# Kernel optimization log

Hardware: AMD Instinct MI355X
Metric: run time of the kernel (lower is better)

The kernel has to match this reference:

```python
import jax, jax.numpy as jnp
import numpy as np

D_MODEL = 1024
N_HEADS = 16
D_K = D_MODEL // N_HEADS
THETA = 10000.0
BATCH, SEQ = 4, 2048


def apply_rope(x, pos, theta=THETA):
    # x: [B, H, S, d_k]; pos: [S] int. Rotate interleaved pairs (x_{2i}, x_{2i+1}).
    half = x.shape[-1] // 2
    inv_freq = theta ** (-jnp.arange(half, dtype=x.dtype) * 2.0 / x.shape[-1])  # [half]
    ang = pos.astype(x.dtype)[:, None] * inv_freq[None, :]                      # [S, half]
    cos, sin = jnp.cos(ang), jnp.sin(ang)
    x1, x2 = x[..., 0::2], x[..., 1::2]
    r1 = x1 * cos - x2 * sin
    r2 = x1 * sin + x2 * cos
    return jnp.stack([r1, r2], axis=-1).reshape(x.shape)


def setup_inputs() -> dict:
    key = jax.random.key(0)
    k1, k2, k3 = jax.random.split(key, 3)
    x = jax.random.normal(k1, (BATCH, SEQ, D_MODEL), dtype=jnp.float32)
    W_qkv = jax.random.normal(k2, (3 * D_MODEL, D_MODEL), dtype=jnp.float32) * (D_MODEL ** -0.5)
    b_qkv = jnp.zeros((3 * D_MODEL,), dtype=jnp.float32)
    W_o = jax.random.normal(k3, (D_MODEL, D_MODEL), dtype=jnp.float32) * (D_MODEL ** -0.5)
    b_o = jnp.zeros((D_MODEL,), dtype=jnp.float32)
    token_positions = jnp.arange(SEQ, dtype=jnp.int64 if jax.config.jax_enable_x64 else jnp.int32)
    return {"x": x, "token_positions": token_positions, "W_qkv": W_qkv,
            "b_qkv": b_qkv, "W_o": W_o, "b_o": b_o}


def reference(x, token_positions, W_qkv, b_qkv, W_o, b_o):
    B, S, _ = x.shape
    qkv = x @ W_qkv.T + b_qkv                                   # [B, S, 3*d_model]
    qkv = qkv.reshape(B, S, 3, N_HEADS, D_K)
    qkv = jnp.transpose(qkv, (2, 0, 3, 1, 4))                   # [3, B, H, S, d_k]
    q, k, v = qkv[0], qkv[1], qkv[2]
    q = apply_rope(q, token_positions)
    k = apply_rope(k, token_positions)
    scores = jnp.einsum('bhqd,bhkd->bhqk', q / jnp.sqrt(jnp.asarray(D_K, x.dtype)), k)
    causal = jnp.tril(jnp.ones((S, S), dtype=bool))             # True where attended
    scores = jnp.where(causal, scores, jnp.asarray(-jnp.inf, scores.dtype))
    attn = jax.nn.softmax(scores, axis=-1)
    out = jnp.einsum('bhqk,bhkd->bhqd', attn, v)                # [B, H, S, d_k]
    out = jnp.transpose(out, (0, 2, 1, 3)).reshape(B, S, D_MODEL)
    return out @ W_o.T + b_o
```

## Files before the change

kernel.cpp:

```cpp
#include <hip/hip_runtime.h>
#include <hip/hip_bf16.h>
#include <cstdint>

#define S_LEN 2048
#define NHEAD 16
#define DMODEL 1024

using short8 = __attribute__((ext_vector_type(8))) short;
using f32x4  = __attribute__((ext_vector_type(4))) float;

__device__ __forceinline__ float bf2f(ushort u) {
    return __uint_as_float(((uint32_t)u) << 16);
}
__device__ __forceinline__ ushort f2bf(float f) {
    uint32_t u = __float_as_uint(f);
    u += 0x7FFF + ((u >> 16) & 1);
    return (ushort)(u >> 16);
}
__device__ __forceinline__ uint32_t cvt_pk_bf16(float lo, float hi) {
    uint32_t r;
    asm("v_cvt_pk_bf16_f32 %0, %1, %2" : "=v"(r) : "v"(lo), "v"(hi));
    return r;
}
__device__ __forceinline__ float exp2_(float x) {
    float r; asm("v_exp_f32 %0, %1" : "=v"(r) : "v"(x)); return r;
}
template<int N> __device__ __forceinline__ void vwait() {
    asm volatile("s_waitcnt vmcnt(%0)" :: "n"(N) : "memory");
}

__global__ void k_cast(const float* __restrict__ in, ushort* __restrict__ out, int n4) {
    int i = blockIdx.x * blockDim.x + threadIdx.x;
    if (i < n4) {
        const float4 v = reinterpret_cast<const float4*>(in)[i];
        ushort4 o;
        o.x = f2bf(v.x); o.y = f2bf(v.y); o.z = f2bf(v.z); o.w = f2bf(v.w);
        reinterpret_cast<ushort4*>(out)[i] = o;
    }
}

__device__ __forceinline__ void gl16(const ushort* g, ushort* l) {
    __builtin_amdgcn_global_load_lds(
        (const __attribute__((address_space(1))) void*)g,
        (__attribute__((address_space(3))) void*)l, 16, 0, 0);
}

__global__ __launch_bounds__(512, 2)
void k_gemm256(const ushort* __restrict__ A, const ushort* __restrict__ Bm,
               const float* __restrict__ bias, const int* __restrict__ pos,
               ushort* __restrict__ Qo, ushort* __restrict__ Ko,
               ushort* __restrict__ Vr, int K, int nbn)
{
    __shared__ ushort As[2][16384];
    __shared__ ushort Bs[2][16384];

    const int bid = blockIdx.x;
    const int cpx = gridDim.x >> 3;
    const int wg = (bid & 7) * cpx + (bid >> 3);
    const int bn = (wg % nbn) * 256, bm = (wg / nbn) * 256;
    const int t = threadIdx.x, w = t >> 6, l = t & 63;
    const int wr = w >> 2, wc = w & 3;
    const int lr = l & 15, lg = l >> 4;

    f32x4 acc[8][4] = {};

    auto stage_pair = [&](int kt, int b, int u0) {
        #pragma unroll
        for (int uu = 0; uu < 2; ++uu) {
            const int u = u0 + uu;
            const int e = (u & 3) * 4096 + t * 8;
            const int r = e >> 6;
            const int c = (e & 63) ^ ((r & 7) << 3);
            if (u < 4) gl16(Bm + (size_t)(bn + r) * K + kt * 64 + c, &Bs[b][e]);
            else       gl16(A  + (size_t)(bm + r) * K + kt * 64 + c, &As[b][e]);
        }
    };

    const int NT = K >> 6;

    stage_pair(0, 0, 0); stage_pair(0, 0, 2);
    stage_pair(0, 0, 4); stage_pair(0, 0, 6);
    if (NT > 1) {
        stage_pair(1, 1, 0); stage_pair(1, 1, 2);
        vwait<4>();
    } else {
        vwait<0>();
    }
    __builtin_amdgcn_s_barrier();

    short8 bfr[4][2];

    for (int tt = 0; tt < NT; ++tt) {
        const int b = tt & 1;
        const ushort* Al = As[b];
        const ushort* Bl = Bs[b];

        #pragma unroll
        for (int p = 0; p < 4; ++p) {
            if (p == 0) {
                #pragma unroll
                for (int n = 0; n < 4; ++n) {
                    const int rB = wc * 64 + n * 16 + lr;
                    #pragma unroll
                    for (int kk = 0; kk < 2; ++kk)
                        bfr[n][kk] = *(const short8*)&Bl[rB * 64 + ((kk * 32 + lg * 8) ^ ((rB & 7) << 3))];
                }
            }
            short8 afr[2][2];
            #pragma unroll
            for (int jj = 0; jj < 2; ++jj) {
                const int rA = wr * 16 + 32 * (2 * p + jj) + lr;
                #pragma unroll
                for (int kk = 0; kk < 2; ++kk)
                    afr[jj][kk] = *(const short8*)&Al[rA * 64 + ((kk * 32 + lg * 8) ^ ((rA & 7) << 3))];
            }
            if      (p == 0) { if (tt + 1 < NT) stage_pair(tt + 1, b ^ 1, 4); }
            else if (p == 1) { if (tt + 1 < NT) stage_pair(tt + 1, b ^ 1, 6); }
            else if (p == 2) { if (tt + 2 < NT) stage_pair(tt + 2, b, 0); }
            else             { if (tt + 2 < NT) stage_pair(tt + 2, b, 2); }

            __builtin_amdgcn_s_barrier();
            __builtin_amdgcn_s_setprio(1);
            #pragma unroll
            for (int jj = 0; jj < 2; ++jj)
                #pragma unroll
                for (int n = 0; n < 4; ++n)
                    #pragma unroll
                    for (int kk = 0; kk < 2; ++kk)
                        acc[2 * p + jj][n] = __builtin_amdgcn_mfma_f32_16x16x32_bf16(
                            afr[jj][kk], bfr[n][kk], acc[2 * p + jj][n], 0, 0, 0);
            __builtin_amdgcn_s_setprio(0);
            if (p == 3) {
                if      (tt + 2 < NT) vwait<4>();
                else if (tt + 1 < NT) vwait<0>();
            }
            __builtin_amdgcn_s_barrier();
        }
    }

    const int col0 = bn + wc * 64 + lr;
    float bv[4];
    #pragma unroll
    for (int n = 0; n < 4; ++n) bv[n] = bias[col0 + n * 16];

    const int typ = bn >> 10;
    if (typ < 2) {
        ushort* Out = (typ == 0) ? Qo : Ko;
        const float scl = (typ == 0) ? 0.18033688f : 1.0f;
        const int h = ((bn & 1023) >> 6) + wc;
        float invf[4];
        #pragma unroll
        for (int n = 0; n < 4; ++n)
            invf[n] = exp2_(-(float)(n * 8 + (lr >> 1)) * 0.41524101186092f);
        #pragma unroll
        for (int j = 0; j < 8; ++j) {
            const int row0 = bm + wr * 16 + 32 * j + lg * 4;
            #pragma unroll
            for (int r = 0; r < 4; ++r) {
                const int row = row0 + r;
                const int s = row & 2047;
                const float p = (float)pos[s];
                const size_t obase = ((size_t)((row >> 11) * NHEAD + h) * S_LEN + s) * 64;
                #pragma unroll
                for (int n = 0; n < 4; ++n) {
                    const float v = acc[j][n][r] + bv[n];
                    const float prt = __shfl_xor(v, 1);
                    float sA, cA;
                    __sincosf(p * invf[n], &sA, &cA);
                    const float res = (lr & 1) ? (prt * sA + v * cA)
                                               : (v * cA - prt * sA);
                    Out[obase + n * 16 + lr] = f2bf(res * scl);
                }
            }
        }
    } else {
        const int vcol0 = (bn & 1023) + wc * 64 + lr;
        #pragma unroll
        for (int j = 0; j < 8; ++j) {
            const int row0 = bm + wr * 16 + 32 * j + lg * 4;
            #pragma unroll
            for (int r = 0; r < 4; ++r) {
                const size_t ro = (size_t)(row0 + r) * 1024;
                #pragma unroll
                for (int n = 0; n < 4; ++n)
                    Vr[ro + vcol0 + n * 16] = f2bf(acc[j][n][r] + bv[n]);
            }
        }
    }
}

__global__ __launch_bounds__(256)
void k_vtrans(const ushort* __restrict__ Vr, ushort* __restrict__ Vt)
{
    __shared__ ushort vlds[64][72];
    const int blk = blockIdx.x;
    const int st = blk & 31, bh = blk >> 5;
    const int b = bh >> 4, h = bh & 15;
    const int t = threadIdx.x;
    const int sl = t >> 2, dc = (t & 3) << 4;
    const int s = st * 64 + sl;
    const size_t base = (size_t)(b * S_LEN + s) * 1024 + h * 64 + dc;
    {
        uint4 v0 = *(const uint4*)(Vr + base);
        uint4 v1 = *(const uint4*)(Vr + base + 8);
        *(uint4*)&vlds[sl][dc] = v0;
        *(uint4*)&vlds[sl][dc + 8] = v1;
    }
    __syncthreads();
    {
        const int d = t >> 2, sc0 = (t & 3) << 4;
        union { uint4 u[2]; ushort us[16]; } o;
        #pragma unroll
        for (int j = 0; j < 16; ++j) o.us[j] = vlds[sc0 + j][d];
        ushort* dst = Vt + ((size_t)bh * 64 + d) * S_LEN + st * 64 + sc0;
        *(uint4*)dst = o.u[0];
        *(uint4*)(dst + 8) = o.u[1];
    }
}

__global__ __launch_bounds__(256, 2)
void k_gemm_bt(const ushort* __restrict__ A, const ushort* __restrict__ Bm,
               const float* __restrict__ bias, float* __restrict__ Cout,
               int M, int N, int K)
{
    __shared__ ushort As[128 * 32];
    __shared__ ushort Bs[128 * 32];
    const int t = threadIdx.x;
    const int w = t >> 6, l = t & 63;
    const int lr = l & 15, lg = l >> 4;
    const int bm = blockIdx.y * 128, bn = blockIdx.x * 128;
    const int wr = (w >> 1) * 64, wc = (w & 1) * 64;

    f32x4 acc[4][4] = {};

    const ushort* ag = A + (size_t)(bm + (t >> 2)) * K + (t & 3) * 8;
    const ushort* bg = Bm + (size_t)(bn + (t >> 2)) * K + (t & 3) * 8;
    ushort* asd = &As[t * 8];
    ushort* bsd = &Bs[t * 8];
    const size_t rowskip = (size_t)64 * K;

    for (int k0 = 0; k0 < K; k0 += 32) {
        gl16(ag + k0, asd);
        gl16(ag + rowskip + k0, asd + 2048);
        gl16(bg + k0, bsd);
        gl16(bg + rowskip + k0, bsd + 2048);
        __syncthreads();
        short8 af[4], bf[4];
        #pragma unroll
        for (int m = 0; m < 4; ++m)
            af[m] = *reinterpret_cast<const short8*>(&As[(wr + m * 16 + lr) * 32 + lg * 8]);
        #pragma unroll
        for (int n = 0; n < 4; ++n)
            bf[n] = *reinterpret_cast<const short8*>(&Bs[(wc + n * 16 + lr) * 32 + lg * 8]);
        #pragma unroll
        for (int m = 0; m < 4; ++m)
            #pragma unroll
            for (int n = 0; n < 4; ++n)
                acc[m][n] = __builtin_amdgcn_mfma_f32_16x16x32_bf16(af[m], bf[n], acc[m][n], 0, 0, 0);
        __syncthreads();
    }

    const int col0 = bn + wc + lr;
    float bv[4];
    #pragma unroll
    for (int n = 0; n < 4; ++n) bv[n] = bias[col0 + n * 16];
    #pragma unroll
    for (int m = 0; m < 4; ++m) {
        const int row0 = bm + wr + m * 16 + lg * 4;
        #pragma unroll
        for (int r = 0; r < 4; ++r) {
            const size_t ro = (size_t)(row0 + r) * N;
            #pragma unroll
            for (int n = 0; n < 4; ++n)
                Cout[ro + col0 + n * 16] = acc[m][n][r] + bv[n];
        }
    }
}

__global__ __launch_bounds__(256, 3)
void k_attn(const ushort* __restrict__ Q, const ushort* __restrict__ Kk,
            const ushort* __restrict__ Vt, ushort* __restrict__ O)
{
    __shared__ ushort Ks[2][4096];
    __shared__ ushort Vs[2][4096];
    __shared__ ushort P[4][32][72];

    const int blk = blockIdx.x;
    const int qb = 15 - (blk >> 6);
    const int bh = blk & 63;
    const int b = bh >> 4, h = bh & 15;
    const int t = threadIdx.x, w = t >> 6, l = t & 63;
    const int lr = l & 15, lg = l >> 4;

    const ushort* Kb = Kk + (size_t)bh * S_LEN * 64;
    const ushort* Vb = Vt + (size_t)bh * 64 * S_LEN;
    const ushort* Qb = Q + (size_t)bh * S_LEN * 64;

    const int qbase0 = qb * 128 + w * 16;
    const int qbase1 = qbase0 + 64;

    short8 qf[2][2];
    #pragma unroll
    for (int qg = 0; qg < 2; ++qg)
        #pragma unroll
        for (int dh = 0; dh < 2; ++dh)
            qf[qg][dh] = *(const short8*)(Qb + (size_t)(qbase0 + qg * 64 + lr) * 64 + dh * 32 + lg * 8);

    f32x4 acc[2][4] = {};
    float mx[2] = {-INFINITY, -INFINITY}, ls[2] = {0.f, 0.f};

    const int nt = 2 * qb + 2;

    auto stage = [&](int kb2, int buf) {
        ushort* Kd = Ks[buf]; ushort* Vd = Vs[buf];
        #pragma unroll
        for (int j = 0; j < 2; ++j) {
            const int e = (j * 256 + t) * 8;
            const int row = e >> 6;
            const int col = (e & 63) ^ ((row & 7) << 3);
            gl16(Kb + (size_t)(kb2 + row) * 64 + col, Kd + e);
            gl16(Vb + (size_t)row * S_LEN + kb2 + col, Vd + e);
        }
    };

    stage(0, 0);
    __syncthreads();

    for (int kt = 0; kt < nt; ++kt) {
        const int cur = kt & 1;
        const int kb = kt * 64;
        if (kt + 1 < nt) stage(kb + 64, cur ^ 1);

        const ushort* Kl = Ks[cur];
        short8 kf[4][2];
        #pragma unroll
        for (int i = 0; i < 4; ++i) {
            const int krow = i * 16 + lr, sw = (krow & 7) << 3;
            kf[i][0] = *(const short8*)&Kl[krow * 64 + ((lg * 8) ^ sw)];
            kf[i][1] = *(const short8*)&Kl[krow * 64 + ((32 + lg * 8) ^ sw)];
        }

        auto do_group = [&](int qg, int qbaseg, bool domask) {
            f32x4 st[4] = {};
            __builtin_amdgcn_s_setprio(1);
            #pragma unroll
            for (int i = 0; i < 4; ++i) {
                st[i] = __builtin_amdgcn_mfma_f32_16x16x32_bf16(kf[i][0], qf[qg][0], st[i], 0, 0, 0);
                st[i] = __builtin_amdgcn_mfma_f32_16x16x32_bf16(kf[i][1], qf[qg][1], st[i], 0, 0, 0);
            }
            __builtin_amdgcn_s_setprio(0);
            if (domask) {
                const int qrow = qbaseg + lr;
                #pragma unroll
                for (int i = 0; i < 4; ++i)
                    #pragma unroll
                    for (int r = 0; r < 4; ++r)
                        if (kb + i * 16 + lg * 4 + r > qrow) st[i][r] = -INFINITY;
            }
            float a0 = fmaxf(fmaxf(st[0][0], st[0][1]), fmaxf(st[0][2], st[0][3]));
            float a1 = fmaxf(fmaxf(st[1][0], st[1][1]), fmaxf(st[1][2], st[1][3]));
            float a2 = fmaxf(fmaxf(st[2][0], st[2][1]), fmaxf(st[2][2], st[2][3]));
            float a3 = fmaxf(fmaxf(st[3][0], st[3][1]), fmaxf(st[3][2], st[3][3]));
            float tm = fmaxf(fmaxf(a0, a1), fmaxf(a2, a3));
            tm = fmaxf(tm, __shfl_xor(tm, 16));
            tm = fmaxf(tm, __shfl_xor(tm, 32));
            float mn = mx[qg];
            if (!__all(tm <= mn + 12.0f)) {
                mn = fmaxf(mx[qg], tm);
                const float sc = exp2_(mx[qg] - mn);
                ls[qg] *= sc;
                #pragma unroll
                for (int d = 0; d < 4; ++d)
                    #pragma unroll
                    for (int r = 0; r < 4; ++r) acc[qg][d][r] *= sc;
                mx[qg] = mn;
            }
            float ps = 0.f;
            #pragma unroll
            for (int i = 0; i < 4; ++i) {
                const float e0 = exp2_(st[i][0] - mn);
                const float e1 = exp2_(st[i][1] - mn);
                const float e2 = exp2_(st[i][2] - mn);
                const float e3 = exp2_(st[i][3] - mn);
                ps += (e0 + e1) + (e2 + e3);
                uint2 pk;
                pk.x = cvt_pk_bf16(e0, e1);
                pk.y = cvt_pk_bf16(e2, e3);
                *(uint2*)&P[w][qg * 16 + lr][i * 16 + lg * 4] = pk;
            }
            ps += __shfl_xor(ps, 16);
            ps += __shfl_xor(ps, 32);
            ls[qg] += ps;
        };

        const bool g0 = (kt < nt - 1);
        do_group(1, qbase1, kt == nt - 1);
        if (g0) do_group(0, qbase0, kt == nt - 2);

        short8 pf1[2], pf0[2];
        pf1[0] = *(const short8*)&P[w][16 + lr][lg * 8];
        pf1[1] = *(const short8*)&P[w][16 + lr][32 + lg * 8];
        if (g0) {
            pf0[0] = *(const short8*)&P[w][lr][lg * 8];
            pf0[1] = *(const short8*)&P[w][lr][32 + lg * 8];
        }
        const ushort* Vl = Vs[cur];
        __builtin_amdgcn_s_setprio(1);
        #pragma unroll
        for (int d = 0; d < 4; ++d) {
            const int vrow = d * 16 + lr, sw = (vrow & 7) << 3;
            short8 v0 = *(const short8*)&Vl[vrow * 64 + ((lg * 8) ^ sw)];
            short8 v1 = *(const short8*)&Vl[vrow * 64 + ((32 + lg * 8) ^ sw)];
            acc[1][d] = __builtin_amdgcn_mfma_f32_16x16x32_bf16(v0, pf1[0], acc[1][d], 0, 0, 0);
            acc[1][d] = __builtin_amdgcn_mfma_f32_16x16x32_bf16(v1, pf1[1], acc[1][d], 0, 0, 0);
            if (g0) {
                acc[0][d] = __builtin_amdgcn_mfma_f32_16x16x32_bf16(v0, pf0[0], acc[0][d], 0, 0, 0);
                acc[0][d] = __builtin_amdgcn_mfma_f32_16x16x32_bf16(v1, pf0[1], acc[0][d], 0, 0, 0);
            }
        }
        __builtin_amdgcn_s_setprio(0);
        __syncthreads();
    }

    #pragma unroll
    for (int qg = 0; qg < 2; ++qg) {
        const float inv = 1.f / ls[qg];
        const int q = qbase0 + qg * 64 + lr;
        #pragma unroll
        for (int d = 0; d < 4; ++d) {
            ushort4 ov;
            #pragma unroll
            for (int r = 0; r < 4; ++r) ((ushort*)&ov)[r] = f2bf(acc[qg][d][r] * inv);
            *(ushort4*)&O[((size_t)(b * S_LEN) + q) * 1024 + h * 64 + d * 16 + lg * 4] = ov;
        }
    }
}

extern "C" void kernel_launch(void* const* d_in, const int* in_sizes, int n_in,
                              void* d_out, int out_size, void* d_ws, size_t ws_size,
                              hipStream_t stream)
{
    const float* x    = (const float*)d_in[0];
    const int*   pos  = (const int*)d_in[1];
    const float* Wqkv = (const float*)d_in[2];
    const float* bqkv = (const float*)d_in[3];
    const float* Wo   = (const float*)d_in[4];
    const float* bo   = (const float*)d_in[5];
    float* out = (float*)d_out;

    char* ws = (char*)d_ws;
    ushort* xb   = (ushort*)(ws);
    ushort* wqb  = (ushort*)(ws + 16777216);
    ushort* wob  = (ushort*)(ws + 23068672);
    ushort* Vrb  = (ushort*)(ws + 25165824);
    ushort* Qb   = (ushort*)(ws + 75497472);
    ushort* Kb   = (ushort*)(ws + 92274688);
    ushort* Vtb  = (ushort*)(ws + 109051904);
    ushort* AOb  = (ushort*)(ws + 125829120);

    k_cast<<<8192, 256, 0, stream>>>(x, xb, 2097152);
    k_cast<<<3072, 256, 0, stream>>>(Wqkv, wqb, 786432);
    k_cast<<<1024, 256, 0, stream>>>(Wo, wob, 262144);
    k_gemm256<<<384, 512, 0, stream>>>(xb, wqb, bqkv, pos, Qb, Kb, Vrb, 1024, 12);
    k_vtrans<<<2048, 256, 0, stream>>>(Vrb, Vtb);
    k_attn<<<1024, 256, 0, stream>>>(Qb, Kb, Vtb, AOb);
    k_gemm_bt<<<dim3(8, 64), 256, 0, stream>>>(AOb, wob, bo, out, 8192, 1024, 1024);
}
```

Before: 185.4 us.

## Fuse fp32-to-bf16 cast of x into QKV GEMM staging and use hardware sin/cos

```diff
diff --git a/kernel.cpp b/kernel.cpp
--- a/kernel.cpp
+++ b/kernel.cpp
@@ -24,6 +24,15 @@
 }
 __device__ __forceinline__ float exp2_(float x) {
     float r; asm("v_exp_f32 %0, %1" : "=v"(r) : "v"(x)); return r;
+}
+__device__ __forceinline__ float fract_(float x) {
+    float r; asm("v_fract_f32 %0, %1" : "=v"(r) : "v"(x)); return r;
+}
+__device__ __forceinline__ float sin_rev(float x) {
+    float r; asm("v_sin_f32 %0, %1" : "=v"(r) : "v"(x)); return r;
+}
+__device__ __forceinline__ float cos_rev(float x) {
+    float r; asm("v_cos_f32 %0, %1" : "=v"(r) : "v"(x)); return r;
 }
 template<int N> __device__ __forceinline__ void vwait() {
     asm volatile("s_waitcnt vmcnt(%0)" :: "n"(N) : "memory");
@@ -46,7 +55,7 @@
 }
 
 __global__ __launch_bounds__(512, 2)
-void k_gemm256(const ushort* __restrict__ A, const ushort* __restrict__ Bm,
+void k_gemm256(const float* __restrict__ X, const ushort* __restrict__ Bm,
                const float* __restrict__ bias, const int* __restrict__ pos,
                ushort* __restrict__ Qo, ushort* __restrict__ Ko,
                ushort* __restrict__ Vr, int K, int nbn)
@@ -63,29 +72,50 @@
     const int lr = l & 15, lg = l >> 4;
 
     f32x4 acc[8][4] = {};
-
-    auto stage_pair = [&](int kt, int b, int u0) {
-        #pragma unroll
-        for (int uu = 0; uu < 2; ++uu) {
-            const int u = u0 + uu;
-            const int e = (u & 3) * 4096 + t * 8;
+    float4 av[4][2];
+
+    const int arow = t >> 3;
+    const int acol = (t & 7) * 8;
+
+    auto stageB4 = [&](int kt, int b) {
+        #pragma unroll
+        for (int u = 0; u < 4; ++u) {
+            const int e = u * 4096 + t * 8;
             const int r = e >> 6;
             const int c = (e & 63) ^ ((r & 7) << 3);
-            if (u < 4) gl16(Bm + (size_t)(bn + r) * K + kt * 64 + c, &Bs[b][e]);
-            else       gl16(A  + (size_t)(bm + r) * K + kt * 64 + c, &As[b][e]);
+            gl16(Bm + (size_t)(bn + r) * K + kt * 64 + c, &Bs[b][e]);
         }
     };
+    auto stageA_issue = [&](int kt) {
+        #pragma unroll
+        for (int u = 0; u < 4; ++u) {
+            const float* src = X + (size_t)(bm + u * 64 + arow) * K + kt * 64 + acol;
+            av[u][0] = *(const float4*)(src);
+            av[u][1] = *(const float4*)(src + 4);
+        }
+    };
+    auto stageA_write = [&](int b) {
+        const int cs = acol ^ ((arow & 7) << 3);
+        #pragma unroll
+        for (int u = 0; u < 4; ++u) {
+            uint4 pk;
+            pk.x = cvt_pk_bf16(av[u][0].x, av[u][0].y);
+            pk.y = cvt_pk_bf16(av[u][0].z, av[u][0].w);
+            pk.z = cvt_pk_bf16(av[u][1].x, av[u][1].y);
+            pk.w = cvt_pk_bf16(av[u][1].z, av[u][1].w);
+            *(uint4*)&As[b][u * 4096 + arow * 64 + cs] = pk;
+        }
+    };
 
     const int NT = K >> 6;
 
-    stage_pair(0, 0, 0); stage_pair(0, 0, 2);
-    stage_pair(0, 0, 4); stage_pair(0, 0, 6);
-    if (NT > 1) {
-        stage_pair(1, 1, 0); stage_pair(1, 1, 2);
-        vwait<4>();
-    } else {
-        vwait<0>();
-    }
+    stageA_issue(0);
+    stageB4(0, 0);
+    stageB4(1, 1);
+    vwait<8>();
+    stageA_write(0);
+    asm volatile("s_waitcnt lgkmcnt(0)" ::: "memory");
+    vwait<4>();
     __builtin_amdgcn_s_barrier();
 
     short8 bfr[4][2];
@@ -114,10 +144,15 @@
                 for (int kk = 0; kk < 2; ++kk)
                     afr[jj][kk] = *(const short8*)&Al[rA * 64 + ((kk * 32 + lg * 8) ^ ((rA & 7) << 3))];
             }
-            if      (p == 0) { if (tt + 1 < NT) stage_pair(tt + 1, b ^ 1, 4); }
-            else if (p == 1) { if (tt + 1 < NT) stage_pair(tt + 1, b ^ 1, 6); }
-            else if (p == 2) { if (tt + 2 < NT) stage_pair(tt + 2, b, 0); }
-            else             { if (tt + 2 < NT) stage_pair(tt + 2, b, 2); }
+            if      (p == 0) { if (tt + 1 < NT) stageA_issue(tt + 1); }
+            else if (p == 1) { if (tt + 2 < NT) stageB4(tt + 2, b); }
+            else if (p == 2) {
+                if (tt + 2 < NT) vwait<4>(); else vwait<0>();
+                if (tt + 1 < NT) {
+                    stageA_write(b ^ 1);
+                    asm volatile("s_waitcnt lgkmcnt(0)" ::: "memory");
+                }
+            }
 
             __builtin_amdgcn_s_barrier();
             __builtin_amdgcn_s_setprio(1);
@@ -130,10 +165,6 @@
                         acc[2 * p + jj][n] = __builtin_amdgcn_mfma_f32_16x16x32_bf16(
                             afr[jj][kk], bfr[n][kk], acc[2 * p + jj][n], 0, 0, 0);
             __builtin_amdgcn_s_setprio(0);
-            if (p == 3) {
-                if      (tt + 2 < NT) vwait<4>();
-                else if (tt + 1 < NT) vwait<0>();
-            }
             __builtin_amdgcn_s_barrier();
         }
     }
@@ -148,10 +179,10 @@
         ushort* Out = (typ == 0) ? Qo : Ko;
         const float scl = (typ == 0) ? 0.18033688f : 1.0f;
         const int h = ((bn & 1023) >> 6) + wc;
-        float invf[4];
+        float invf_rev[4];
         #pragma unroll
         for (int n = 0; n < 4; ++n)
-            invf[n] = exp2_(-(float)(n * 8 + (lr >> 1)) * 0.41524101186092f);
+            invf_rev[n] = exp2_(-(float)(n * 8 + (lr >> 1)) * 0.41524101186092f) * 0.15915494309f;
         #pragma unroll
         for (int j = 0; j < 8; ++j) {
             const int row0 = bm + wr * 16 + 32 * j + lg * 4;
@@ -165,8 +196,8 @@
                 for (int n = 0; n < 4; ++n) {
                     const float v = acc[j][n][r] + bv[n];
                     const float prt = __shfl_xor(v, 1);
-                    float sA, cA;
-                    __sincosf(p * invf[n], &sA, &cA);
+                    const float a = fract_(p * invf_rev[n]);
+                    const float sA = sin_rev(a), cA = cos_rev(a);
                     const float res = (lr & 1) ? (prt * sA + v * cA)
                                                : (v * cA - prt * sA);
                     Out[obase + n * 16 + lr] = f2bf(res * scl);
@@ -449,19 +480,17 @@
     float* out = (float*)d_out;
 
     char* ws = (char*)d_ws;
-    ushort* xb   = (ushort*)(ws);
-    ushort* wqb  = (ushort*)(ws + 16777216);
-    ushort* wob  = (ushort*)(ws + 23068672);
-    ushort* Vrb  = (ushort*)(ws + 25165824);
-    ushort* Qb   = (ushort*)(ws + 75497472);
-    ushort* Kb   = (ushort*)(ws + 92274688);
-    ushort* Vtb  = (ushort*)(ws + 109051904);
-    ushort* AOb  = (ushort*)(ws + 125829120);
-
-    k_cast<<<8192, 256, 0, stream>>>(x, xb, 2097152);
+    ushort* wqb  = (ushort*)(ws);
+    ushort* wob  = (ushort*)(ws + 6291456);
+    ushort* Vrb  = (ushort*)(ws + 8388608);
+    ushort* Qb   = (ushort*)(ws + 25165824);
+    ushort* Kb   = (ushort*)(ws + 41943040);
+    ushort* Vtb  = (ushort*)(ws + 58720256);
+    ushort* AOb  = (ushort*)(ws + 75497472);
+
     k_cast<<<3072, 256, 0, stream>>>(Wqkv, wqb, 786432);
     k_cast<<<1024, 256, 0, stream>>>(Wo, wob, 262144);
-    k_gemm256<<<384, 512, 0, stream>>>(xb, wqb, bqkv, pos, Qb, Kb, Vrb, 1024, 12);
+    k_gemm256<<<384, 512, 0, stream>>>(x, wqb, bqkv, pos, Qb, Kb, Vrb, 1024, 12);
     k_vtrans<<<2048, 256, 0, stream>>>(Vrb, Vtb);
     k_attn<<<1024, 256, 0, stream>>>(Qb, Kb, Vtb, AOb);
     k_gemm_bt<<<dim3(8, 64), 256, 0, stream>>>(AOb, wob, bo, out, 8192, 1024, 1024);
```

After: 202.5 us. 9.3% more time.
